# Performance work log

Measured on AMD Instinct MI355X. Metric: run time of the kernel, lower is better.

The kernel has to match this reference:

```python
import jax, jax.numpy as jnp
import numpy as np

N_NODES = 500_000
N_FEAT = 125          # embedding dim; cat with pos(3) -> 128
HIDDEN = 128
OUT_DIM = 64
N_TYPES = 100
N_GRAPHS = 4096


def setup_inputs() -> dict:
    key = jax.random.key(0)
    ks = jax.random.split(key, 10)
    pos = jax.random.normal(ks[0], (N_NODES, 3), dtype=jnp.float32)
    z = jax.random.randint(ks[1], (N_NODES,), 0, N_TYPES)
    batch = jnp.sort(jax.random.randint(ks[2], (N_NODES,), 0, N_GRAPHS))
    emb = jax.random.normal(ks[3], (N_TYPES, N_FEAT), dtype=jnp.float32)
    s1 = 1.0 / np.sqrt(N_FEAT + 3)
    s2 = 1.0 / np.sqrt(HIDDEN)
    W1 = jax.random.normal(ks[4], (N_FEAT + 3, HIDDEN), dtype=jnp.float32) * s1
    b1 = jnp.zeros((HIDDEN,), dtype=jnp.float32)
    W2 = jax.random.normal(ks[5], (HIDDEN, HIDDEN), dtype=jnp.float32) * s2
    b2 = jnp.zeros((HIDDEN,), dtype=jnp.float32)
    W3 = jax.random.normal(ks[6], (HIDDEN, OUT_DIM), dtype=jnp.float32) * s2
    b3 = jnp.zeros((OUT_DIM,), dtype=jnp.float32)
    return {"pos": pos, "z": z, "batch": batch, "emb": emb,
            "W1": W1, "b1": b1, "W2": W2, "b2": b2, "W3": W3, "b3": b3}


def reference(pos, z, batch, emb, W1, b1, W2, b2, W3, b3):
    # embed node types and concat with 3D positions  -> [N, 128]
    x = jnp.concatenate([pos, emb[z]], axis=-1)
    # two equivariant-transformer layers (per-node transform) + relu
    x = jax.nn.relu(x @ W1 + b1)   # [N, H]
    x = jax.nn.relu(x @ W2 + b2)   # [N, H]
    # output head
    x = x @ W3 + b3                # [N, O]
    # global mean pool per graph
    s = jax.ops.segment_sum(x, batch, num_segments=N_GRAPHS)                    # [G, O]
    cnt = jax.ops.segment_sum(jnp.ones((x.shape[0], 1), x.dtype), batch,
                              num_segments=N_GRAPHS)                            # [G, 1]
    return s / jnp.maximum(cnt, 1.0)
```

## Files before the change

### kernel.cpp

```cpp
#include <hip/hip_runtime.h>
#include <hip/hip_bf16.h>

#define N_NODES 500000
#define N_FEAT 125
#define HID 128
#define OUTD 64
#define N_GRAPHS 4096
#define N_TYPES 100
#define WTILE 32
#define NBLOCKS 256
#define NTHREADS 512
#define NWAVES 8
#define WPAD 136
#define OPADF 68
#define NSLOTS 40
#define EPAD 132

typedef float f32x4 __attribute__((ext_vector_type(4)));
typedef float f32x2 __attribute__((ext_vector_type(2)));
typedef short s16x8 __attribute__((ext_vector_type(8)));

#define OFF_W2 0
#define OFF_W3 (OFF_W2 + HID * WPAD * 2)
#define OFF_B2 (OFF_W3 + OUTD * WPAD * 2)
#define OFF_T  (OFF_B2 + HID * 4)
#define OFF_SCR (OFF_T + N_TYPES * WPAD * 2)
#define SCR_BYTES (WTILE * WPAD * 2)
#define OFF_SLOT (OFF_SCR + NWAVES * SCR_BYTES)
#define OFF_CNT (OFF_SLOT + NSLOTS * OUTD * 4)
#define OFF_IDS (OFF_CNT + NSLOTS * 4)
#define LDS_BYTES (OFF_IDS + NWAVES * WTILE * 4)

__device__ __forceinline__ unsigned short f2bf(float f) {
  union { float f; unsigned u; } v; v.f = f;
  unsigned r = v.u + 0x7FFFu + ((v.u >> 16) & 1u);
  return (unsigned short)(r >> 16);
}
__device__ __forceinline__ unsigned pk2bf(float a, float b) {
  __hip_bfloat162 h = __float22bfloat162_rn(float2{a, b});
  union { __hip_bfloat162 h; unsigned u; } v; v.h = h;
  return v.u;
}
__device__ __forceinline__ f32x2 unpk_bf2(unsigned u) {
  union { unsigned u; float f; } lo, hi;
  lo.u = u << 16; hi.u = u & 0xffff0000u;
  return (f32x2){lo.f, hi.f};
}

__device__ __forceinline__ void wavefence() {
  __builtin_amdgcn_sched_barrier(0);
  __builtin_amdgcn_wave_barrier();
  __builtin_amdgcn_sched_barrier(0);
}

extern "C" __global__ void __launch_bounds__(NTHREADS, 2)
gnn_all(const float* __restrict__ pos, const int* __restrict__ z,
        const int* __restrict__ batch, const float* __restrict__ emb,
        const float* __restrict__ W1, const float* __restrict__ b1,
        const float* __restrict__ W2, const float* __restrict__ b2,
        const float* __restrict__ W3, const float* __restrict__ b3,
        float* __restrict__ out)
{
  extern __shared__ char lds[];
  unsigned short* w2t = (unsigned short*)(lds + OFF_W2);
  unsigned short* w3t = (unsigned short*)(lds + OFF_W3);
  float* bias2 = (float*)(lds + OFF_B2);
  unsigned short* Tl = (unsigned short*)(lds + OFF_T);
  float* embs = (float*)(lds + OFF_SCR);
  float* slotsum = (float*)(lds + OFF_SLOT);
  int* slotcnt = (int*)(lds + OFF_CNT);

  const int t = threadIdx.x, b = blockIdx.x;
  const int wave = t >> 6, lane = t & 63, quad = lane >> 4, l15 = lane & 15;

  const int tlo = 61 * b + (b < 9 ? b : 9);
  const int ntl = 61 + (b < 9 ? 1 : 0);
  const int start_node = tlo * WTILE;
  const int end_node = start_node + ntl * WTILE;

  for (int i = t; i < HID * HID; i += NTHREADS) {
    int k = i >> 7, n = i & 127;
    w2t[n * WPAD + k] = f2bf(W2[i]);
  }
  for (int i = t; i < HID * OUTD; i += NTHREADS) {
    int k = i >> 6, n = i & 63;
    w3t[n * WPAD + k] = f2bf(W3[i]);
  }
  for (int i = t; i < N_TYPES * EPAD; i += NTHREADS) {
    int g = i / EPAD, k = i - g * EPAD;
    embs[i] = (k < N_FEAT) ? emb[g * N_FEAT + k] : 0.f;
  }
  if (t < HID) bias2[t] = b2[t];

  for (int i = t; i < NSLOTS * OUTD; i += NTHREADS) slotsum[i] = 0.f;
  if (t < NSLOTS) slotcnt[t] = 0;

  const int slot_base = batch[start_node];
  const int prev_g = (b == 0) ? -1 : batch[start_node - 1];
  const int own_hi = batch[end_node - 1];
  int n_ext = 0;
  if (end_node < N_NODES) {
    int probe = -1;
    if (lane < 12 && end_node + lane * WTILE < N_NODES)
      probe = batch[end_node + lane * WTILE];
    unsigned long long m = __ballot(probe == own_hi);
    n_ext = (int)__builtin_ctzll(~m);
    if (n_ext == 12) {
      while (end_node + WTILE * n_ext < N_NODES &&
             batch[end_node + WTILE * n_ext] == own_hi) ++n_ext;
    }
  }

  f32x2 w1r2[3][4][4];
  #pragma unroll
  for (int c = 0; c < 3; ++c)
    #pragma unroll
    for (int k = 0; k < 4; ++k)
      #pragma unroll
      for (int p = 0; p < 4; ++p)
        w1r2[c][k][p] = *(const f32x2*)&W1[c * HID + k * 32 + quad * 8 + 2 * p];
  const float b3l = b3[lane];

  s16x8 afr[4];
  {
    const int jt = wave;
    #pragma unroll
    for (int kf = 0; kf < 4; ++kf) {
      s16x8 fr;
      #pragma unroll
      for (int u = 0; u < 8; ++u) {
        const int k = kf * 32 + quad * 8 + u;
        float v = (k < N_FEAT) ? W1[(3 + k) * HID + jt * 16 + l15] : 0.f;
        fr[u] = (short)f2bf(v);
      }
      afr[kf] = fr;
    }
  }

  __syncthreads();

  {
    const int jt = wave;
    const int j0 = jt * 16 + quad * 4;
    const f32x4 b1v = *(const f32x4*)&b1[j0];

    for (int gt = 0; gt < 7; ++gt) {
      const int g = gt * 16 + l15;
      const int gg = (g < N_TYPES) ? g : (N_TYPES - 1);
      const float* erow = embs + gg * EPAD;
      f32x4 acc = {};
      #pragma unroll
      for (int kf = 0; kf < 4; ++kf) {
        const int k0 = kf * 32 + quad * 8;
        f32x4 e0 = *(const f32x4*)(erow + k0);
        f32x4 e1 = *(const f32x4*)(erow + k0 + 4);
        s16x8 bf;
        ((unsigned*)&bf)[0] = pk2bf(e0[0], e0[1]);
        ((unsigned*)&bf)[1] = pk2bf(e0[2], e0[3]);
        ((unsigned*)&bf)[2] = pk2bf(e1[0], e1[1]);
        ((unsigned*)&bf)[3] = pk2bf(e1[2], e1[3]);
        acc = __builtin_amdgcn_mfma_f32_16x16x32_bf16(afr[kf], bf, acc, 0, 0, 0);
      }
      if (g < N_TYPES) {
        unsigned lo = pk2bf(acc[0] + b1v[0], acc[1] + b1v[1]);
        unsigned hi = pk2bf(acc[2] + b1v[2], acc[3] + b1v[3]);
        *(uint2*)(Tl + g * WPAD + j0) = uint2{lo, hi};
      }
    }
  }

  unsigned short* xs = (unsigned short*)(lds + OFF_SCR + wave * SCR_BYTES);
  float* xo = (float*)xs;
  int* ids = (int*)(lds + OFF_IDS) + wave * WTILE;

  __syncthreads();

  const int ntot = ntl + n_ext;
  for (int j = wave; j < ntot; j += NWAVES) {
    const int base = start_node + j * WTILE;

    if (lane < WTILE) ids[lane] = batch[base + lane];

    s16x8 a[2][4];
    #pragma unroll
    for (int m = 0; m < 2; ++m) {
      const int node = base + m * 16 + l15;
      const int zi = z[node];
      const f32x2 px2 = {pos[node * 3], pos[node * 3]};
      const f32x2 py2 = {pos[node * 3 + 1], pos[node * 3 + 1]};
      const f32x2 pz2 = {pos[node * 3 + 2], pos[node * 3 + 2]};
      const unsigned short* Tr = Tl + zi * WPAD;
      #pragma unroll
      for (int k = 0; k < 4; ++k) {
        s16x8 tf = *(const s16x8*)(Tr + k * 32 + quad * 8);
        s16x8 fr;
        #pragma unroll
        for (int p = 0; p < 4; ++p) {
          f32x2 tv = unpk_bf2(((const unsigned*)&tf)[p]);
          tv = __builtin_elementwise_fma(px2, w1r2[0][k][p], tv);
          tv = __builtin_elementwise_fma(py2, w1r2[1][k][p], tv);
          tv = __builtin_elementwise_fma(pz2, w1r2[2][k][p], tv);
          tv = __builtin_elementwise_max(tv, (f32x2){0.f, 0.f});
          ((unsigned*)&fr)[p] = pk2bf(tv[0], tv[1]);
        }
        a[m][k] = fr;
      }
    }

    f32x4 acc[8][2] = {};
    #pragma unroll
    for (int oi = 0; oi < 8; ++oi)
      #pragma unroll
      for (int k = 0; k < 4; ++k) {
        s16x8 w = *(const s16x8*)(w2t + (oi * 16 + l15) * WPAD + k * 32 + quad * 8);
        acc[oi][0] = __builtin_amdgcn_mfma_f32_16x16x32_bf16(w, a[0][k], acc[oi][0], 0, 0, 0);
        acc[oi][1] = __builtin_amdgcn_mfma_f32_16x16x32_bf16(w, a[1][k], acc[oi][1], 0, 0, 0);
      }
    #pragma unroll
    for (int oi = 0; oi < 8; ++oi) {
      const int f0 = oi * 16 + quad * 4;
      f32x4 bv = *(const f32x4*)(bias2 + f0);
      #pragma unroll
      for (int m = 0; m < 2; ++m) {
        f32x4 s = acc[oi][m] + bv;
        s = __builtin_elementwise_max(s, (f32x4){0.f, 0.f, 0.f, 0.f});
        unsigned lo = pk2bf(s[0], s[1]);
        unsigned hi = pk2bf(s[2], s[3]);
        *(uint2*)(xs + (m * 16 + l15) * WPAD + f0) = uint2{lo, hi};
      }
    }
    wavefence();
    #pragma unroll
    for (int m = 0; m < 2; ++m)
      #pragma unroll
      for (int k = 0; k < 4; ++k)
        a[m][k] = *(const s16x8*)(xs + (m * 16 + l15) * WPAD + k * 32 + quad * 8);
    wavefence();

    f32x4 acc3[4][2] = {};
    #pragma unroll
    for (int oi = 0; oi < 4; ++oi)
      #pragma unroll
      for (int k = 0; k < 4; ++k) {
        s16x8 w = *(const s16x8*)(w3t + (oi * 16 + l15) * WPAD + k * 32 + quad * 8);
        acc3[oi][0] = __builtin_amdgcn_mfma_f32_16x16x32_bf16(w, a[0][k], acc3[oi][0], 0, 0, 0);
        acc3[oi][1] = __builtin_amdgcn_mfma_f32_16x16x32_bf16(w, a[1][k], acc3[oi][1], 0, 0, 0);
      }
    #pragma unroll
    for (int oi = 0; oi < 4; ++oi)
      #pragma unroll
      for (int m = 0; m < 2; ++m)
        *(f32x4*)(xo + (m * 16 + l15) * OPADF + oi * 16 + quad * 4) = acc3[oi][m];
    wavefence();

    {
      int cur = ids[0];
      float run = 0.f; int rc = 0;
      #pragma unroll 1
      for (int n = 0; n < WTILE; ++n) {
        int bb2 = ids[n];
        if (bb2 != cur) {
          if (cur != prev_g && cur <= own_hi) {
            atomicAdd(&slotsum[(cur - slot_base) * OUTD + lane], run);
            if (lane == 0) atomicAdd(&slotcnt[cur - slot_base], rc);
          }
          run = 0.f; rc = 0; cur = bb2;
        }
        run += xo[n * OPADF + lane]; rc++;
      }
      if (cur != prev_g && cur <= own_hi) {
        atomicAdd(&slotsum[(cur - slot_base) * OUTD + lane], run);
        if (lane == 0) atomicAdd(&slotcnt[cur - slot_base], rc);
      }
    }
    wavefence();
  }

  __syncthreads();

  const int own_lo = slot_base + (slot_base == prev_g ? 1 : 0);
  for (int g = own_lo + wave; g <= own_hi; g += NWAVES) {
    int s = g - slot_base;
    float sum = slotsum[s * OUTD + lane];
    int c = slotcnt[s];
    out[g * OUTD + lane] = (c > 0) ? (sum / (float)c + b3l) : 0.f;
  }
  const int next_g = (end_node < N_NODES) ? batch[end_node] : N_GRAPHS;
  for (int g = own_hi + 1 + wave; g < next_g; g += NWAVES)
    out[g * OUTD + lane] = 0.f;
  if (b == 0)
    for (int g = wave; g < slot_base; g += NWAVES)
      out[g * OUTD + lane] = 0.f;
}

extern "C" void kernel_launch(void* const* d_in, const int* in_sizes, int n_in,
                              void* d_out, int out_size, void* d_ws, size_t ws_size,
                              hipStream_t stream) {
  const float* pos  = (const float*)d_in[0];
  const int*   z    = (const int*)d_in[1];
  const int*   batch= (const int*)d_in[2];
  const float* emb  = (const float*)d_in[3];
  const float* W1   = (const float*)d_in[4];
  const float* b1   = (const float*)d_in[5];
  const float* W2   = (const float*)d_in[6];
  const float* b2   = (const float*)d_in[7];
  const float* W3   = (const float*)d_in[8];
  const float* b3   = (const float*)d_in[9];

  hipFuncSetAttribute((const void*)gnn_all,
                      hipFuncAttributeMaxDynamicSharedMemorySize, LDS_BYTES);

  hipLaunchKernelGGL(gnn_all, dim3(NBLOCKS), dim3(NTHREADS), LDS_BYTES, stream,
                     pos, z, batch, emb, W1, b1, W2, b2, W3, b3, (float*)d_out);
}
```

Before: 151.1 us.

## Permute W2 output columns so layer-2 results feed layer-3 MFMA in registers

Result: no change. 150.7 us (-0.3%).

```diff
diff --git a/kernel.cpp b/kernel.cpp
--- a/kernel.cpp
+++ b/kernel.cpp
@@ -25,11 +25,15 @@
 #define OFF_B2 (OFF_W3 + OUTD * WPAD * 2)
 #define OFF_T  (OFF_B2 + HID * 4)
 #define OFF_SCR (OFF_T + N_TYPES * WPAD * 2)
-#define SCR_BYTES (WTILE * WPAD * 2)
+#define SCR_BYTES (WTILE * OPADF * 4)
 #define OFF_SLOT (OFF_SCR + NWAVES * SCR_BYTES)
 #define OFF_CNT (OFF_SLOT + NSLOTS * OUTD * 4)
 #define OFF_IDS (OFF_CNT + NSLOTS * 4)
 #define LDS_BYTES (OFF_IDS + NWAVES * WTILE * 4)
+
+__device__ __forceinline__ int fperm(int n) {
+  return ((n >> 5) << 5) + ((n >> 2) & 3) * 8 + ((n >> 4) & 1) * 4 + (n & 3);
+}
 
 __device__ __forceinline__ unsigned short f2bf(float f) {
   union { float f; unsigned u; } v; v.f = f;
@@ -80,7 +84,7 @@
 
   for (int i = t; i < HID * HID; i += NTHREADS) {
     int k = i >> 7, n = i & 127;
-    w2t[n * WPAD + k] = f2bf(W2[i]);
+    w2t[n * WPAD + k] = f2bf(W2[k * HID + fperm(n)]);
   }
   for (int i = t; i < HID * OUTD; i += NTHREADS) {
     int k = i >> 6, n = i & 63;
@@ -90,7 +94,7 @@
     int g = i / EPAD, k = i - g * EPAD;
     embs[i] = (k < N_FEAT) ? emb[g * N_FEAT + k] : 0.f;
   }
-  if (t < HID) bias2[t] = b2[t];
+  if (t < HID) bias2[t] = b2[fperm(t)];
 
   for (int i = t; i < NSLOTS * OUTD; i += NTHREADS) slotsum[i] = 0.f;
   if (t < NSLOTS) slotcnt[t] = 0;
@@ -169,11 +173,17 @@
     }
   }
 
-  unsigned short* xs = (unsigned short*)(lds + OFF_SCR + wave * SCR_BYTES);
-  float* xo = (float*)xs;
+  float* xo = (float*)(lds + OFF_SCR + wave * SCR_BYTES);
   int* ids = (int*)(lds + OFF_IDS) + wave * WTILE;
 
   __syncthreads();
+
+  s16x8 w3f[4][4];
+  #pragma unroll
+  for (int oi = 0; oi < 4; ++oi)
+    #pragma unroll
+    for (int kf = 0; kf < 4; ++kf)
+      w3f[oi][kf] = *(const s16x8*)(w3t + (oi * 16 + l15) * WPAD + kf * 32 + quad * 8);
 
   const int ntot = ntl + n_ext;
   for (int j = wave; j < ntot; j += NWAVES) {
@@ -207,44 +217,41 @@
       }
     }
 
-    f32x4 acc[8][2] = {};
-    #pragma unroll
-    for (int oi = 0; oi < 8; ++oi)
-      #pragma unroll
-      for (int k = 0; k < 4; ++k) {
-        s16x8 w = *(const s16x8*)(w2t + (oi * 16 + l15) * WPAD + k * 32 + quad * 8);
-        acc[oi][0] = __builtin_amdgcn_mfma_f32_16x16x32_bf16(w, a[0][k], acc[oi][0], 0, 0, 0);
-        acc[oi][1] = __builtin_amdgcn_mfma_f32_16x16x32_bf16(w, a[1][k], acc[oi][1], 0, 0, 0);
-      }
-    #pragma unroll
-    for (int oi = 0; oi < 8; ++oi) {
-      const int f0 = oi * 16 + quad * 4;
-      f32x4 bv = *(const f32x4*)(bias2 + f0);
+    s16x8 a3[2][4];
+    #pragma unroll
+    for (int p = 0; p < 4; ++p) {
+      f32x4 acc2[2][2] = {};
+      #pragma unroll
+      for (int kf = 0; kf < 4; ++kf) {
+        s16x8 w0 = *(const s16x8*)(w2t + ((2 * p) * 16 + l15) * WPAD + kf * 32 + quad * 8);
+        s16x8 w1f = *(const s16x8*)(w2t + ((2 * p + 1) * 16 + l15) * WPAD + kf * 32 + quad * 8);
+        acc2[0][0] = __builtin_amdgcn_mfma_f32_16x16x32_bf16(w0, a[0][kf], acc2[0][0], 0, 0, 0);
+        acc2[0][1] = __builtin_amdgcn_mfma_f32_16x16x32_bf16(w0, a[1][kf], acc2[0][1], 0, 0, 0);
+        acc2[1][0] = __builtin_amdgcn_mfma_f32_16x16x32_bf16(w1f, a[0][kf], acc2[1][0], 0, 0, 0);
+        acc2[1][1] = __builtin_amdgcn_mfma_f32_16x16x32_bf16(w1f, a[1][kf], acc2[1][1], 0, 0, 0);
+      }
+      const f32x4 bv0 = *(const f32x4*)(bias2 + (2 * p) * 16 + quad * 4);
+      const f32x4 bv1 = *(const f32x4*)(bias2 + (2 * p + 1) * 16 + quad * 4);
       #pragma unroll
       for (int m = 0; m < 2; ++m) {
-        f32x4 s = acc[oi][m] + bv;
-        s = __builtin_elementwise_max(s, (f32x4){0.f, 0.f, 0.f, 0.f});
-        unsigned lo = pk2bf(s[0], s[1]);
-        unsigned hi = pk2bf(s[2], s[3]);
-        *(uint2*)(xs + (m * 16 + l15) * WPAD + f0) = uint2{lo, hi};
-      }
-    }
-    wavefence();
-    #pragma unroll
-    for (int m = 0; m < 2; ++m)
-      #pragma unroll
-      for (int k = 0; k < 4; ++k)
-        a[m][k] = *(const s16x8*)(xs + (m * 16 + l15) * WPAD + k * 32 + quad * 8);
-    wavefence();
+        f32x4 s0 = __builtin_elementwise_max(acc2[0][m] + bv0, (f32x4){0.f, 0.f, 0.f, 0.f});
+        f32x4 s1 = __builtin_elementwise_max(acc2[1][m] + bv1, (f32x4){0.f, 0.f, 0.f, 0.f});
+        s16x8 fr;
+        ((unsigned*)&fr)[0] = pk2bf(s0[0], s0[1]);
+        ((unsigned*)&fr)[1] = pk2bf(s0[2], s0[3]);
+        ((unsigned*)&fr)[2] = pk2bf(s1[0], s1[1]);
+        ((unsigned*)&fr)[3] = pk2bf(s1[2], s1[3]);
+        a3[m][p] = fr;
+      }
+    }
 
     f32x4 acc3[4][2] = {};
     #pragma unroll
     for (int oi = 0; oi < 4; ++oi)
       #pragma unroll
-      for (int k = 0; k < 4; ++k) {
-        s16x8 w = *(const s16x8*)(w3t + (oi * 16 + l15) * WPAD + k * 32 + quad * 8);
-        acc3[oi][0] = __builtin_amdgcn_mfma_f32_16x16x32_bf16(w, a[0][k], acc3[oi][0], 0, 0, 0);
-        acc3[oi][1] = __builtin_amdgcn_mfma_f32_16x16x32_bf16(w, a[1][k], acc3[oi][1], 0, 0, 0);
+      for (int kf = 0; kf < 4; ++kf) {
+        acc3[oi][0] = __builtin_amdgcn_mfma_f32_16x16x32_bf16(w3f[oi][kf], a3[0][kf], acc3[oi][0], 0, 0, 0);
+        acc3[oi][1] = __builtin_amdgcn_mfma_f32_16x16x32_bf16(w3f[oi][kf], a3[1][kf], acc3[oi][1], 0, 0, 0);
       }
     #pragma unroll
     for (int oi = 0; oi < 4; ++oi)
```
